# Performance work log

Measured on AMD Instinct MI355X. Metric: run time of the kernel, lower is better.

Reference implementation:

```python
import jax, jax.numpy as jnp
import numpy as np

NU = 100000
NV = 100000
D = 128
R = 5          # num_support (rating levels)
O = 64         # output_dim // num_support
E = 640000     # edges per relation


def setup_inputs() -> dict:
    key = jax.random.key(0)
    ks = jax.random.split(key, 7)
    x_u = jax.random.normal(ks[0], (NU, D), dtype=jnp.float32)
    x_v = jax.random.normal(ks[1], (NV, D), dtype=jnp.float32)
    sup_rows = jax.random.randint(ks[2], (R, E), 0, NU, dtype=jnp.int32)
    sup_cols = jax.random.randint(ks[3], (R, E), 0, NV, dtype=jnp.int32)
    sup_vals = jax.random.uniform(ks[4], (R, E), dtype=jnp.float32)
    weights_u = jax.random.normal(ks[5], (R, D, O), dtype=jnp.float32)
    weights_v = jax.random.normal(ks[6], (R, D, O), dtype=jnp.float32)
    return {"x_u": x_u, "x_v": x_v, "sup_rows": sup_rows, "sup_cols": sup_cols,
            "sup_vals": sup_vals, "weights_u": weights_u, "weights_v": weights_v}


def _spmm(rows, cols, vals, feat, num_segments):
    # sparse [num_segments, n_src] @ feat [n_src, O] via gather + segment_sum
    return jax.ops.segment_sum(vals[:, None] * feat[cols], rows,
                               num_segments=num_segments)


def reference(x_u, x_v, sup_rows, sup_cols, sup_vals, weights_u, weights_v):
    # ordinal weight accumulation: wu_i = sum_{j<=i} weights_u[j]
    Wu = jnp.cumsum(weights_u, axis=0)  # [R, D, O]
    Wv = jnp.cumsum(weights_v, axis=0)  # [R, D, O]
    tmp_u = jnp.einsum('nd,rdo->rno', x_u, Wu)  # [R, NU, O]
    tmp_v = jnp.einsum('md,rdo->rmo', x_v, Wv)  # [R, NV, O]
    # z_u = sum_r support[r] @ tmp_v[r];  z_v = sum_r support[r]^T @ tmp_u[r]
    z_u = jax.vmap(lambda r, c, v, f: _spmm(r, c, v, f, NU))(
        sup_rows, sup_cols, sup_vals, tmp_v).sum(axis=0)
    z_v = jax.vmap(lambda r, c, v, f: _spmm(r, c, v, f, NV))(
        sup_cols, sup_rows, sup_vals, tmp_u).sum(axis=0)
    return jax.nn.relu(z_u), jax.nn.relu(z_v)
```

## Files before the change

kernel.cpp:

```cpp
#include <hip/hip_runtime.h>
#include <hip/hip_bf16.h>

#define R_SUP 5
#define D_IN 128
#define O_OUT 64
#define NBMAX 512
#define CHUNK 4096
#define FCAP 4608

typedef __attribute__((ext_vector_type(8))) short bf16x8;
typedef __attribute__((ext_vector_type(4))) float f32x4;

__device__ __forceinline__ unsigned short f2bf(float f) {
  union { float f; unsigned int u; } c; c.f = f;
  unsigned int u = c.u;
  return (unsigned short)((u + 0x7FFFu + ((u >> 16) & 1u)) >> 16);
}
__device__ __forceinline__ float bf2f(unsigned short h) {
  return __uint_as_float(((unsigned int)h) << 16);
}

__global__ __launch_bounds__(256) void cumsum_w(
    const float* __restrict__ wu, const float* __restrict__ wv,
    float* __restrict__ wcu, float* __restrict__ wcv,
    unsigned short* __restrict__ wtbu, unsigned short* __restrict__ wtbv) {
  int i = blockIdx.x * 256 + threadIdx.x;
  if (i >= D_IN * O_OUT) return;
  const int d = i >> 6;
  const int o = i & 63;
  float su = 0.f, sv = 0.f;
#pragma unroll
  for (int r = 0; r < R_SUP; ++r) {
    su += wu[r * D_IN * O_OUT + i];
    sv += wv[r * D_IN * O_OUT + i];
    wcu[r * D_IN * O_OUT + i] = su;
    wcv[r * D_IN * O_OUT + i] = sv;
    wtbu[((size_t)r * O_OUT + o) * D_IN + d] = f2bf(su);
    wtbv[((size_t)r * O_OUT + o) * D_IN + d] = f2bf(sv);
  }
}

__global__ __launch_bounds__(256) void zero_f32(float* __restrict__ p, int n4) {
  int i = blockIdx.x * 256 + threadIdx.x;
  int stride = gridDim.x * 256;
  float4 z = make_float4(0.f, 0.f, 0.f, 0.f);
  for (; i < n4; i += stride) ((float4*)p)[i] = z;
}

__global__ __launch_bounds__(256) void zero_i32(int* __restrict__ p, int n) {
  int i = blockIdx.x * 256 + threadIdx.x;
  int stride = gridDim.x * 256;
  for (; i < n; i += stride) p[i] = 0;
}

__global__ __launch_bounds__(256) void gemm5_mfma(
    const float* __restrict__ x,
    const unsigned short* __restrict__ wtb,
    unsigned short* __restrict__ tmp5, size_t strideR, int N) {
  __shared__ unsigned short st[64][72];
  const int tid = threadIdx.x;
  const int row0 = blockIdx.x * 64;
  const int wave = tid >> 6;
  const int lane = tid & 63;
  const int m = lane & 15;
  const int q = lane >> 4;
  const int o0 = wave * 16;

  bf16x8 a[4][4];
#pragma unroll
  for (int rt = 0; rt < 4; ++rt) {
    int row = row0 + rt * 16 + m;
    if (row >= N) row = N - 1;
    const float* px = x + (size_t)row * D_IN + q * 8;
#pragma unroll
    for (int k0 = 0; k0 < 4; ++k0) {
      float4 f0 = *(const float4*)(px + k0 * 32);
      float4 f1 = *(const float4*)(px + k0 * 32 + 4);
      bf16x8 t;
      t[0] = (short)f2bf(f0.x); t[1] = (short)f2bf(f0.y);
      t[2] = (short)f2bf(f0.z); t[3] = (short)f2bf(f0.w);
      t[4] = (short)f2bf(f1.x); t[5] = (short)f2bf(f1.y);
      t[6] = (short)f2bf(f1.z); t[7] = (short)f2bf(f1.w);
      a[rt][k0] = t;
    }
  }

  const int rr = tid >> 2;
  const int c0 = (tid & 3) * 16;

  for (int r = 0; r < R_SUP; ++r) {
    bf16x8 b[4];
    const unsigned short* pw =
        wtb + ((size_t)r * O_OUT + o0 + m) * D_IN + q * 8;
#pragma unroll
    for (int k0 = 0; k0 < 4; ++k0)
      b[k0] = *(const bf16x8*)(pw + k0 * 32);
#pragma unroll
    for (int rt = 0; rt < 4; ++rt) {
      f32x4 acc = {0.f, 0.f, 0.f, 0.f};
#pragma unroll
      for (int k0 = 0; k0 < 4; ++k0)
        acc = __builtin_amdgcn_mfma_f32_16x16x32_bf16(a[rt][k0], b[k0], acc,
                                                      0, 0, 0);
#pragma unroll
      for (int reg = 0; reg < 4; ++reg)
        st[rt * 16 + q * 4 + reg][o0 + m] = f2bf(acc[reg]);
    }
    __syncthreads();
    if (row0 + rr < N) {
      unsigned short* pz = tmp5 + (size_t)r * strideR + (size_t)row0 * O_OUT;
      *(int4*)(pz + rr * O_OUT + c0) = *(const int4*)&st[rr][c0];
      *(int4*)(pz + rr * O_OUT + c0 + 8) = *(const int4*)&st[rr][c0 + 8];
    }
    __syncthreads();
  }
}

__global__ __launch_bounds__(256) void coarse_hist(
    const int* __restrict__ rows, const int* __restrict__ cols,
    int* __restrict__ cnt_u, int* __restrict__ cnt_v, int nE5,
    int nbu, int nbv) {
  __shared__ int hu[NBMAX], hv[NBMAX];
  const int tid = threadIdx.x;
  for (int t = tid; t < NBMAX; t += 256) { hu[t] = 0; hv[t] = 0; }
  __syncthreads();
  const int n4 = nE5 >> 2;
  int i = blockIdx.x * 256 + tid;
  int stride = gridDim.x * 256;
  for (; i < n4; i += stride) {
    int4 rr = ((const int4*)rows)[i];
    int4 cc = ((const int4*)cols)[i];
    atomicAdd(&hu[rr.x >> 8], 1); atomicAdd(&hu[rr.y >> 8], 1);
    atomicAdd(&hu[rr.z >> 8], 1); atomicAdd(&hu[rr.w >> 8], 1);
    atomicAdd(&hv[cc.x >> 8], 1); atomicAdd(&hv[cc.y >> 8], 1);
    atomicAdd(&hv[cc.z >> 8], 1); atomicAdd(&hv[cc.w >> 8], 1);
  }
  for (i = (n4 << 2) + blockIdx.x * 256 + tid; i < nE5; i += stride) {
    atomicAdd(&hu[rows[i] >> 8], 1);
    atomicAdd(&hv[cols[i] >> 8], 1);
  }
  __syncthreads();
  for (int t = tid; t < nbu; t += 256) if (hu[t]) atomicAdd(&cnt_u[t], hu[t]);
  for (int t = tid; t < nbv; t += 256) if (hv[t]) atomicAdd(&cnt_v[t], hv[t]);
}

__global__ __launch_bounds__(512) void coarse_scan(
    int* __restrict__ cnt_u, int* __restrict__ cnt_v,
    int* __restrict__ cb_u, int* __restrict__ cb_v,
    int* __restrict__ gcur_u, int* __restrict__ gcur_v, int nbu, int nbv) {
  int* cnt = blockIdx.x ? cnt_v : cnt_u;
  int* cb  = blockIdx.x ? cb_v  : cb_u;
  int* gc  = blockIdx.x ? gcur_v : gcur_u;
  int nb   = blockIdx.x ? nbv   : nbu;
  __shared__ int sc[NBMAX];
  const int t = threadIdx.x;
  sc[t] = (t < nb) ? cnt[t] : 0;
  __syncthreads();
  for (int off = 1; off < NBMAX; off <<= 1) {
    int add = (t >= off) ? sc[t - off] : 0;
    __syncthreads();
    sc[t] += add;
    __syncthreads();
  }
  int excl = t ? sc[t - 1] : 0;
  if (t < nb) { cb[t] = excl; gc[t] = excl; }
  if (t == 0) cb[nb] = sc[NBMAX - 1];
}

__global__ __launch_bounds__(512) void coarse_scatter(
    const int* __restrict__ rows, const int* __restrict__ cols,
    const float* __restrict__ vals, int* __restrict__ gcur_u,
    int* __restrict__ gcur_v, int2* __restrict__ mid_u,
    int2* __restrict__ mid_v, int nE5, int E, int nbu, int nbv) {
  __shared__ int2 buf[CHUNK];
  __shared__ int h[NBMAX], sc[NBMAX], gb[NBMAX], cur[NBMAX];
  const int tid = threadIdx.x;
  const int dir = blockIdx.x & 1;
  const int base = (blockIdx.x >> 1) * CHUNK;
  const int end = min(base + CHUNK, nE5);
  const int E2 = 2 * E, E3 = 3 * E, E4 = 4 * E;

  const int* ids   = dir ? cols : rows;
  const int* other = dir ? rows : cols;
  int* gcur = dir ? gcur_v : gcur_u;
  int2* mid = dir ? mid_v : mid_u;
  const int nb = dir ? nbv : nbu;

  h[tid] = 0;
  __syncthreads();
  for (int i = base + tid; i < end; i += 512)
    atomicAdd(&h[ids[i] >> 8], 1);
  __syncthreads();
  sc[tid] = h[tid];
  __syncthreads();
  for (int off = 1; off < NBMAX; off <<= 1) {
    int add = (tid >= off) ? sc[tid - off] : 0;
    __syncthreads();
    sc[tid] += add;
    __syncthreads();
  }
  int excl = tid ? sc[tid - 1] : 0;
  cur[tid] = excl;
  if (tid < nb && h[tid]) gb[tid] = atomicAdd(&gcur[tid], h[tid]);
  __syncthreads();
  for (int i = base + tid; i < end; i += 512) {
    int id = ids[i];
    int src = other[i];
    int vb = __float_as_int(vals[i]);
    int r = (i >= E) + (i >= E2) + (i >= E3) + (i >= E4);
    int pos = atomicAdd(&cur[id >> 8], 1);
    buf[pos] = make_int2(((id & 255) << 20) | (r << 17) | src, vb);
  }
  __syncthreads();
  const int wv = tid >> 6;
  const int lane = tid & 63;
  for (int b = wv; b < nb; b += 8) {
    int s = b ? sc[b - 1] : 0;
    int e = sc[b];
    if (s == e) continue;
    int2* dst = mid + gb[b];
    for (int j = s + lane; j < e; j += 64) dst[j - s] = buf[j];
  }
}

__global__ __launch_bounds__(512) void spmm_sorted(
    const int2* __restrict__ mid, const int* __restrict__ cb,
    const unsigned short* __restrict__ tmp5, float* __restrict__ z,
    int Ndst, int strideR) {
  __shared__ int2 buf[FCAP];
  __shared__ int sc[256], cur[256];
  const int tid = threadIdx.x;
  const int b = blockIdx.x;
  const int s = cb[b];
  const int e = cb[b + 1];
  const int d0 = b * 256;
  const int gid = tid >> 4;
  const int lane = tid & 15;
  const unsigned short* tl = tmp5 + lane * 4;

  float4 acc[8];
#pragma unroll
  for (int k = 0; k < 8; ++k) acc[k] = make_float4(0.f, 0.f, 0.f, 0.f);

  for (int cs = s; cs < e; cs += FCAP) {
    const int ce = min(cs + FCAP, e);
    if (tid < 256) sc[tid] = 0;
    __syncthreads();
    for (int i = cs + tid; i < ce; i += 512)
      atomicAdd(&sc[(mid[i].x >> 20) & 255], 1);
    __syncthreads();
    for (int off = 1; off < 256; off <<= 1) {
      int add = (tid < 256 && tid >= off) ? sc[tid - off] : 0;
      __syncthreads();
      if (tid < 256) sc[tid] += add;
      __syncthreads();
    }
    if (tid < 256) cur[tid] = tid ? sc[tid - 1] : 0;
    __syncthreads();
    for (int i = cs + tid; i < ce; i += 512) {
      int2 pk = mid[i];
      int dl = (pk.x >> 20) & 255;
      int r = (pk.x >> 17) & 7;
      int src = pk.x & 0x1FFFF;
      int pos = atomicAdd(&cur[dl], 1);
      buf[pos] = make_int2(r * strideR + (src << 6), pk.y);
    }
    __syncthreads();
#pragma unroll
    for (int k = 0; k < 8; ++k) {
      const int dl = gid + (k << 5);
      int i = dl ? sc[dl - 1] : 0;
      const int re = sc[dl];
      float4 a = acc[k];
      for (; i + 8 <= re; i += 8) {
        int2 pk[8];
#pragma unroll
        for (int j = 0; j < 8; ++j) pk[j] = buf[i + j];
        ushort4 hh[8];
#pragma unroll
        for (int j = 0; j < 8; ++j)
          hh[j] = *(const ushort4*)(tl + (unsigned)pk[j].x);
#pragma unroll
        for (int j = 0; j < 8; ++j) {
          float v = __int_as_float(pk[j].y);
          a.x += v * bf2f(hh[j].x);
          a.y += v * bf2f(hh[j].y);
          a.z += v * bf2f(hh[j].z);
          a.w += v * bf2f(hh[j].w);
        }
      }
      for (; i < re; ++i) {
        int2 pk = buf[i];
        float v = __int_as_float(pk.y);
        ushort4 hh = *(const ushort4*)(tl + (unsigned)pk.x);
        a.x += v * bf2f(hh.x);
        a.y += v * bf2f(hh.y);
        a.z += v * bf2f(hh.z);
        a.w += v * bf2f(hh.w);
      }
      acc[k] = a;
    }
    __syncthreads();
  }
#pragma unroll
  for (int k = 0; k < 8; ++k) {
    int d = d0 + gid + (k << 5);
    if (d < Ndst) {
      float4 o;
      o.x = fmaxf(acc[k].x, 0.f);
      o.y = fmaxf(acc[k].y, 0.f);
      o.z = fmaxf(acc[k].z, 0.f);
      o.w = fmaxf(acc[k].w, 0.f);
      ((float4*)(z + (size_t)d * O_OUT))[lane] = o;
    }
  }
}

__global__ __launch_bounds__(256) void gemm64(
    const float* __restrict__ x, const float* __restrict__ w,
    float* __restrict__ out, int N) {
  __shared__ float sXT[D_IN][68];
  __shared__ float sW[D_IN][O_OUT];
  const int tid = threadIdx.x;
  const int row0 = blockIdx.x * 64;
  for (int i = tid; i < 2048; i += 256) {
    int d = i >> 4;
    int o4 = i & 15;
    ((float4*)&sW[d][0])[o4] = ((const float4*)w)[i];
  }
  for (int i = tid; i < 2048; i += 256) {
    int rl = i >> 5;
    int d4 = i & 31;
    int row = row0 + rl;
    float4 xv = make_float4(0.f, 0.f, 0.f, 0.f);
    if (row < N) xv = ((const float4*)x)[(size_t)row * 32 + d4];
    sXT[d4 * 4 + 0][rl] = xv.x;
    sXT[d4 * 4 + 1][rl] = xv.y;
    sXT[d4 * 4 + 2][rl] = xv.z;
    sXT[d4 * 4 + 3][rl] = xv.w;
  }
  __syncthreads();
  const int col4 = (tid & 15) * 4;
  const int row4 = (tid >> 4) * 4;
  float acc[4][4] = {};
#pragma unroll 8
  for (int d = 0; d < D_IN; ++d) {
    float4 xv = *(const float4*)&sXT[d][row4];
    float4 wv = *(const float4*)&sW[d][col4];
    acc[0][0] += xv.x * wv.x; acc[0][1] += xv.x * wv.y; acc[0][2] += xv.x * wv.z; acc[0][3] += xv.x * wv.w;
    acc[1][0] += xv.y * wv.x; acc[1][1] += xv.y * wv.y; acc[1][2] += xv.y * wv.z; acc[1][3] += xv.y * wv.w;
    acc[2][0] += xv.z * wv.x; acc[2][1] += xv.z * wv.y; acc[2][2] += xv.z * wv.z; acc[2][3] += xv.z * wv.w;
    acc[3][0] += xv.w * wv.x; acc[3][1] += xv.w * wv.y; acc[3][2] += xv.w * wv.z; acc[3][3] += xv.w * wv.w;
  }
#pragma unroll
  for (int i = 0; i < 4; ++i) {
    int row = row0 + row4 + i;
    if (row < N)
      *(float4*)&out[row * O_OUT + col4] =
          make_float4(acc[i][0], acc[i][1], acc[i][2], acc[i][3]);
  }
}

__global__ __launch_bounds__(256) void spmm_push(
    const int* __restrict__ dst, const int* __restrict__ src,
    const float* __restrict__ vals, const float* __restrict__ tmp,
    float* __restrict__ z, int E) {
  int t = blockIdx.x * 256 + threadIdx.x;
  int e = t >> 4;
  int lane = t & 15;
  if (e >= E) return;
  int d_ = dst[e];
  int s_ = src[e];
  float v = vals[e];
  float4 f = ((const float4*)tmp)[s_ * 16 + lane];
  float* zp = z + (size_t)d_ * O_OUT + lane * 4;
  atomicAdd(zp + 0, v * f.x);
  atomicAdd(zp + 1, v * f.y);
  atomicAdd(zp + 2, v * f.z);
  atomicAdd(zp + 3, v * f.w);
}

__global__ __launch_bounds__(256) void relu_f32(float* __restrict__ p, int n4) {
  int i = blockIdx.x * 256 + threadIdx.x;
  int stride = gridDim.x * 256;
  for (; i < n4; i += stride) {
    float4 v = ((float4*)p)[i];
    v.x = v.x > 0.f ? v.x : 0.f;
    v.y = v.y > 0.f ? v.y : 0.f;
    v.z = v.z > 0.f ? v.z : 0.f;
    v.w = v.w > 0.f ? v.w : 0.f;
    ((float4*)p)[i] = v;
  }
}

extern "C" void kernel_launch(void* const* d_in, const int* in_sizes, int n_in,
                              void* d_out, int out_size, void* d_ws, size_t ws_size,
                              hipStream_t stream) {
  const float* x_u      = (const float*)d_in[0];
  const float* x_v      = (const float*)d_in[1];
  const int*   sup_rows = (const int*)d_in[2];
  const int*   sup_cols = (const int*)d_in[3];
  const float* sup_vals = (const float*)d_in[4];
  const float* wu       = (const float*)d_in[5];
  const float* wv       = (const float*)d_in[6];

  const int NU = in_sizes[0] / D_IN;
  const int NV = in_sizes[1] / D_IN;
  const int E  = in_sizes[2] / R_SUP;
  const int Nmax = NU > NV ? NU : NV;
  const int nE5 = R_SUP * E;
  const int nbu = (NU + 255) / 256;
  const int nbv = (NV + 255) / 256;
  const int nbmax = nbu > nbv ? nbu : nbv;

  float* out = (float*)d_out;
  float* z_u = out;
  float* z_v = out + (size_t)NU * O_OUT;

  const int WDO = R_SUP * D_IN * O_OUT;
  const size_t strideR = (size_t)Nmax * O_OUT;
  const size_t bpad = (size_t)nbmax + 16;

  const size_t mid_bytes = (((size_t)nE5 * 8) + 255) & ~(size_t)255;

  const size_t needR = 2 * mid_bytes + strideR * R_SUP * 2 +
                       (size_t)2 * WDO * 4 + (size_t)2 * WDO * 2 +
                       6 * bpad * 4 + 512;

  if (ws_size >= needR && nbmax <= NBMAX && Nmax < (1 << 17)) {
    char* base = (char*)d_ws;
    int2* mid_u = (int2*)base;
    int2* mid_v = (int2*)(base + mid_bytes);
    unsigned short* tmp5 = (unsigned short*)(base + 2 * mid_bytes);
    float* wcu = (float*)(tmp5 + strideR * R_SUP);
    float* wcv = wcu + WDO;
    unsigned short* wtbu = (unsigned short*)(wcv + WDO);
    unsigned short* wtbv = wtbu + WDO;
    int* cnt_u = (int*)(wtbv + WDO);
    int* cnt_v = cnt_u + bpad;
    int* cb_u  = cnt_v + bpad;
    int* cb_v  = cb_u + bpad;
    int* gcur_u = cb_v + bpad;
    int* gcur_v = gcur_u + bpad;

    cumsum_w<<<(D_IN * O_OUT + 255) / 256, 256, 0, stream>>>(
        wu, wv, wcu, wcv, wtbu, wtbv);
    zero_i32<<<(2 * (int)bpad + 255) / 256, 256, 0, stream>>>(cnt_u, 2 * (int)bpad);
    coarse_hist<<<512, 256, 0, stream>>>(sup_rows, sup_cols, cnt_u, cnt_v,
                                         nE5, nbu, nbv);
    coarse_scan<<<2, 512, 0, stream>>>(cnt_u, cnt_v, cb_u, cb_v, gcur_u,
                                       gcur_v, nbu, nbv);
    coarse_scatter<<<2 * ((nE5 + CHUNK - 1) / CHUNK), 512, 0, stream>>>(
        sup_rows, sup_cols, sup_vals, gcur_u, gcur_v, mid_u, mid_v, nE5, E,
        nbu, nbv);

    gemm5_mfma<<<(NV + 63) / 64, 256, 0, stream>>>(x_v, wtbv, tmp5, strideR, NV);
    spmm_sorted<<<nbu, 512, 0, stream>>>(mid_u, cb_u, tmp5, z_u, NU,
                                         (int)strideR);

    gemm5_mfma<<<(NU + 63) / 64, 256, 0, stream>>>(x_u, wtbu, tmp5, strideR, NU);
    spmm_sorted<<<nbv, 512, 0, stream>>>(mid_v, cb_v, tmp5, z_v, NV,
                                         (int)strideR);
  } else {
    float* wcu = (float*)d_ws;
    float* wcv = wcu + WDO;
    unsigned short* wtbu = (unsigned short*)(wcv + WDO);
    unsigned short* wtbv = wtbu + WDO;
    float* tmp = (float*)(wtbv + WDO);
    const int n4_out = out_size / 4;
    cumsum_w<<<(D_IN * O_OUT + 255) / 256, 256, 0, stream>>>(
        wu, wv, wcu, wcv, wtbu, wtbv);
    zero_f32<<<1024, 256, 0, stream>>>(out, n4_out);
    const int spmm_blocks = (E * 16 + 255) / 256;
    for (int r = 0; r < R_SUP; ++r) {
      const int* rws = sup_rows + (size_t)r * E;
      const int* cls = sup_cols + (size_t)r * E;
      const float* vls = sup_vals + (size_t)r * E;
      gemm64<<<(NV + 63) / 64, 256, 0, stream>>>(x_v, wcv + r * D_IN * O_OUT, tmp, NV);
      spmm_push<<<spmm_blocks, 256, 0, stream>>>(rws, cls, vls, tmp, z_u, E);
      gemm64<<<(NU + 63) / 64, 256, 0, stream>>>(x_u, wcu + r * D_IN * O_OUT, tmp, NU);
      spmm_push<<<spmm_blocks, 256, 0, stream>>>(cls, rws, vls, tmp, z_v, E);
    }
    relu_f32<<<1024, 256, 0, stream>>>(out, n4_out);
  }
}
```

Measured before the change: 495.3 us.

## Merge the u and v GEMM and SpMM passes into dual-side kernels, enlarge chunks

Adds gemm5_dual and spmm_dual, which process both the user and item sides in one launch by splitting the grid on block index. Each side gets its own bf16 tmp buffer when the workspace is large enough. This removes two launches and the serialisation between the passes, and gives each launch a fuller grid (spmm goes from about 391 to 782 blocks). Separately, CHUNK and FCAP are doubled, so the scatter and spmm shared buffers grow to roughly 72KB of LDS per block, which may lower occupancy. The dual path needs an extra tmp5-sized workspace and falls back to the old sequence otherwise.

```diff
diff --git a/kernel.cpp b/kernel.cpp
--- a/kernel.cpp
+++ b/kernel.cpp
@@ -5,8 +5,8 @@
 #define D_IN 128
 #define O_OUT 64
 #define NBMAX 512
-#define CHUNK 4096
-#define FCAP 4608
+#define CHUNK 8192
+#define FCAP 9216
 
 typedef __attribute__((ext_vector_type(8))) short bf16x8;
 typedef __attribute__((ext_vector_type(4))) float f32x4;
@@ -53,13 +53,11 @@
   for (; i < n; i += stride) p[i] = 0;
 }
 
-__global__ __launch_bounds__(256) void gemm5_mfma(
-    const float* __restrict__ x,
-    const unsigned short* __restrict__ wtb,
-    unsigned short* __restrict__ tmp5, size_t strideR, int N) {
-  __shared__ unsigned short st[64][72];
+__device__ __forceinline__ void gemm5_body(
+    const float* __restrict__ x, const unsigned short* __restrict__ wtb,
+    unsigned short* __restrict__ tmp5, size_t strideR, int N, int row0,
+    unsigned short (*st)[72]) {
   const int tid = threadIdx.x;
-  const int row0 = blockIdx.x * 64;
   const int wave = tid >> 6;
   const int lane = tid & 63;
   const int m = lane & 15;
@@ -114,6 +112,27 @@
     }
     __syncthreads();
   }
+}
+
+__global__ __launch_bounds__(256) void gemm5_mfma(
+    const float* __restrict__ x, const unsigned short* __restrict__ wtb,
+    unsigned short* __restrict__ tmp5, size_t strideR, int N) {
+  __shared__ unsigned short st[64][72];
+  gemm5_body(x, wtb, tmp5, strideR, N, blockIdx.x * 64, st);
+}
+
+__global__ __launch_bounds__(256) void gemm5_dual(
+    const float* __restrict__ xv, const float* __restrict__ xu,
+    const unsigned short* __restrict__ wtbv,
+    const unsigned short* __restrict__ wtbu,
+    unsigned short* __restrict__ t5B, unsigned short* __restrict__ t5A,
+    size_t strideR, int NV, int NU, int gv) {
+  __shared__ unsigned short st[64][72];
+  const int bi = blockIdx.x;
+  if (bi < gv)
+    gemm5_body(xv, wtbv, t5B, strideR, NV, bi * 64, st);
+  else
+    gemm5_body(xu, wtbu, t5A, strideR, NU, (bi - gv) * 64, st);
 }
 
 __global__ __launch_bounds__(256) void coarse_hist(
@@ -223,14 +242,11 @@
   }
 }
 
-__global__ __launch_bounds__(512) void spmm_sorted(
+__device__ __forceinline__ void spmm_body(
     const int2* __restrict__ mid, const int* __restrict__ cb,
     const unsigned short* __restrict__ tmp5, float* __restrict__ z,
-    int Ndst, int strideR) {
-  __shared__ int2 buf[FCAP];
-  __shared__ int sc[256], cur[256];
+    int Ndst, int strideR, int b, int2* buf, int* sc, int* cur) {
   const int tid = threadIdx.x;
-  const int b = blockIdx.x;
   const int s = cb[b];
   const int e = cb[b + 1];
   const int d0 = b * 256;
@@ -316,6 +332,31 @@
   }
 }
 
+__global__ __launch_bounds__(512) void spmm_sorted(
+    const int2* __restrict__ mid, const int* __restrict__ cb,
+    const unsigned short* __restrict__ tmp5, float* __restrict__ z,
+    int Ndst, int strideR) {
+  __shared__ int2 buf[FCAP];
+  __shared__ int sc[256], cur[256];
+  spmm_body(mid, cb, tmp5, z, Ndst, strideR, blockIdx.x, buf, sc, cur);
+}
+
+__global__ __launch_bounds__(512) void spmm_dual(
+    const int2* __restrict__ mid_u, const int2* __restrict__ mid_v,
+    const int* __restrict__ cb_u, const int* __restrict__ cb_v,
+    const unsigned short* __restrict__ t5B,
+    const unsigned short* __restrict__ t5A,
+    float* __restrict__ out, int NU, int NV, int nbu, int strideR) {
+  __shared__ int2 buf[FCAP];
+  __shared__ int sc[256], cur[256];
+  const int bi = blockIdx.x;
+  if (bi < nbu)
+    spmm_body(mid_u, cb_u, t5B, out, NU, strideR, bi, buf, sc, cur);
+  else
+    spmm_body(mid_v, cb_v, t5A, out + (size_t)NU * O_OUT, NV, strideR,
+              bi - nbu, buf, sc, cur);
+}
+
 __global__ __launch_bounds__(256) void gemm64(
     const float* __restrict__ x, const float* __restrict__ w,
     float* __restrict__ out, int N) {
@@ -422,17 +463,23 @@
   const size_t bpad = (size_t)nbmax + 16;
 
   const size_t mid_bytes = (((size_t)nE5 * 8) + 255) & ~(size_t)255;
-
-  const size_t needR = 2 * mid_bytes + strideR * R_SUP * 2 +
-                       (size_t)2 * WDO * 4 + (size_t)2 * WDO * 2 +
+  const size_t t5_bytes = (strideR * R_SUP * 2 + 255) & ~(size_t)255;
+
+  const size_t fixed = (size_t)2 * WDO * 4 + (size_t)2 * WDO * 2 +
                        6 * bpad * 4 + 512;
-
-  if (ws_size >= needR && nbmax <= NBMAX && Nmax < (1 << 17)) {
+  const size_t need2 = 2 * mid_bytes + 2 * t5_bytes + fixed;
+  const size_t need1 = 2 * mid_bytes + t5_bytes + fixed;
+
+  if (ws_size >= need1 && nbmax <= NBMAX && Nmax < (1 << 17)) {
+    const bool dual = (ws_size >= need2);
     char* base = (char*)d_ws;
     int2* mid_u = (int2*)base;
     int2* mid_v = (int2*)(base + mid_bytes);
-    unsigned short* tmp5 = (unsigned short*)(base + 2 * mid_bytes);
-    float* wcu = (float*)(tmp5 + strideR * R_SUP);
+    unsigned short* t5B = (unsigned short*)(base + 2 * mid_bytes);
+    unsigned short* t5A = dual ? (unsigned short*)(base + 2 * mid_bytes + t5_bytes)
+                               : t5B;
+    char* tail = (char*)(base + 2 * mid_bytes + (dual ? 2 : 1) * t5_bytes);
+    float* wcu = (float*)tail;
     float* wcv = wcu + WDO;
     unsigned short* wtbu = (unsigned short*)(wcv + WDO);
     unsigned short* wtbv = wtbu + WDO;
@@ -454,13 +501,22 @@
         sup_rows, sup_cols, sup_vals, gcur_u, gcur_v, mid_u, mid_v, nE5, E,
         nbu, nbv);
 
-    gemm5_mfma<<<(NV + 63) / 64, 256, 0, stream>>>(x_v, wtbv, tmp5, strideR, NV);
-    spmm_sorted<<<nbu, 512, 0, stream>>>(mid_u, cb_u, tmp5, z_u, NU,
-                                         (int)strideR);
-
-    gemm5_mfma<<<(NU + 63) / 64, 256, 0, stream>>>(x_u, wtbu, tmp5, strideR, NU);
-    spmm_sorted<<<nbv, 512, 0, stream>>>(mid_v, cb_v, tmp5, z_v, NV,
-                                         (int)strideR);
+    if (dual) {
+      const int gv = (NV + 63) / 64;
+      const int gu = (NU + 63) / 64;
+      gemm5_dual<<<gv + gu, 256, 0, stream>>>(x_v, x_u, wtbv, wtbu, t5B, t5A,
+                                              strideR, NV, NU, gv);
+      spmm_dual<<<nbu + nbv, 512, 0, stream>>>(mid_u, mid_v, cb_u, cb_v, t5B,
+                                               t5A, out, NU, NV, nbu,
+                                               (int)strideR);
+    } else {
+      gemm5_mfma<<<(NV + 63) / 64, 256, 0, stream>>>(x_v, wtbv, t5B, strideR, NV);
+      spmm_sorted<<<nbu, 512, 0, stream>>>(mid_u, cb_u, t5B, z_u, NU,
+                                           (int)strideR);
+      gemm5_mfma<<<(NU + 63) / 64, 256, 0, stream>>>(x_u, wtbu, t5B, strideR, NU);
+      spmm_sorted<<<nbv, 512, 0, stream>>>(mid_v, cb_v, t5B, z_v, NV,
+                                           (int)strideR);
+    }
   } else {
     float* wcu = (float*)d_ws;
     float* wcv = wcu + WDO;
```

New measurement: 501.1 us. About the same (+1.2%).
